# Performance work log

Hardware: AMD Instinct MI355X
Metric: run time of the kernel (lower is better)

The kernel has to match this reference:

```python
import jax, jax.numpy as jnp
import numpy as np

NUM_HEADS = 1
HIDDEN = 256
HEAD_DIM = HIDDEN // NUM_HEADS
SCALE = HEAD_DIM ** -0.5


def _rotate_pairwise(x):
    # (... , d) -> rotate adjacent pairs: (x0,x1,x2,x3,..) -> (-x1,x0,-x3,x2,..)
    shape = x.shape
    x = x.reshape(*shape[:-1], -1, 2)
    x = jnp.stack([-x[..., 1], x[..., 0]], axis=-1)
    return x.reshape(shape)


def setup_inputs() -> dict:
    key = jax.random.key(0)
    ks = jax.random.split(key, 12)
    B, PB, QS, KS = 1, 1, 4096, 16448
    KV_IN = 64
    d = {
        'query': jax.random.normal(ks[0], (B, PB, QS, HIDDEN), jnp.float32),
        'key': jax.random.normal(ks[1], (B, PB, KS, KV_IN), jnp.float32),
        'value': jax.random.normal(ks[2], (B, PB, KS, KV_IN), jnp.float32),
        'rope_cos': jax.random.normal(ks[3], (QS, HEAD_DIM), jnp.float32),
        'rope_sin': jax.random.normal(ks[4], (QS, HEAD_DIM), jnp.float32),
        'wq': jax.random.normal(ks[5], (HIDDEN, HIDDEN), jnp.float32) * (HIDDEN ** -0.5),
        'bq': jnp.zeros((HIDDEN,), jnp.float32),
        'wk': jax.random.normal(ks[6], (KV_IN, HIDDEN), jnp.float32) * (KV_IN ** -0.5),
        'bk': jnp.zeros((HIDDEN,), jnp.float32),
        'wv': jax.random.normal(ks[7], (KV_IN, HIDDEN), jnp.float32) * (KV_IN ** -0.5),
        'bv': jnp.zeros((HIDDEN,), jnp.float32),
        'wo': jax.random.normal(ks[8], (HIDDEN, HIDDEN), jnp.float32) * (HIDDEN ** -0.5),
        'bo': jnp.zeros((HIDDEN,), jnp.float32),
        'num_k_exclude_rope': 64,
    }
    return d


def reference(query, key, value, rope_cos, rope_sin, wq, bq, wk, bk, wv, bv, wo, bo, num_k_exclude_rope):
    batch, pb, qs, _ = query.shape
    ks = key.shape[2]
    B = batch * pb
    # projections -> [B, H, S, hd]
    q = (query @ wq + bq).reshape(B, qs, NUM_HEADS, HEAD_DIM).transpose(0, 2, 1, 3)
    k = (key @ wk + bk).reshape(B, ks, NUM_HEADS, HEAD_DIM).transpose(0, 2, 1, 3)
    v = (value @ wv + bv).reshape(B, ks, NUM_HEADS, HEAD_DIM).transpose(0, 2, 1, 3)
    cos = rope_cos[None, None]  # [1,1,QS,hd]
    sin = rope_sin[None, None]
    # split off non-RoPE keys (object pointer tokens)
    n_rot = ks - num_k_exclude_rope
    k_rot, k_pass = k[:, :, :n_rot, :], k[:, :, n_rot:, :]
    q = q * cos + _rotate_pairwise(q) * sin
    if n_rot != qs:  # rope_k_repeat branch (static shapes)
        rep = n_rot // qs
        cos_k = jnp.repeat(cos, rep, axis=2)
        sin_k = jnp.repeat(sin, rep, axis=2)
    else:
        cos_k, sin_k = cos, sin
    k_emb = k_rot * cos_k + _rotate_pairwise(k_rot) * sin_k
    k = jnp.concatenate([k_emb, k_pass], axis=-2)
    attn = jax.nn.softmax(jnp.einsum('bhqd,bhkd->bhqk', q * SCALE, k), axis=-1)
    x = jnp.einsum('bhqk,bhkd->bhqd', attn, v)
    x = x.transpose(0, 2, 1, 3).reshape(batch, pb, qs, HIDDEN)
    return x @ wo + bo
```

## Files before the change

### kernel.cpp

```cpp
#include <hip/hip_runtime.h>
#include <hip/hip_bf16.h>

typedef __attribute__((ext_vector_type(4))) float floatx4;
typedef __attribute__((ext_vector_type(8))) short shortx8;
typedef __attribute__((ext_vector_type(8))) _Float16 halfx8;
typedef _Float16 half_t;

#define MFMA_BF16(A,B,C) __builtin_amdgcn_mfma_f32_16x16x32_bf16((A),(B),(C),0,0,0)
#define GLOBAL_AS __attribute__((address_space(1)))
#define LDS_AS __attribute__((address_space(3)))

static __device__ __forceinline__ unsigned short f2b(float f) {
    union { float f; unsigned u; } v; v.f = f;
    unsigned r = v.u + 0x7FFFu + ((v.u >> 16) & 1u);
    return (unsigned short)(r >> 16);
}
static __device__ __forceinline__ unsigned pack_bf16(float lo, float hi) {
    return (unsigned)f2b(lo) | ((unsigned)f2b(hi) << 16);
}
static __device__ __forceinline__ unsigned pack_half(float lo, float hi) {
    union { half_t h[2]; unsigned u; } p;
    p.h[0] = (half_t)lo; p.h[1] = (half_t)hi;
    return p.u;
}
static __device__ __forceinline__ unsigned cvtpk_bf16(float lo, float hi) {
    unsigned r;
    asm("v_cvt_pk_bf16_f32 %0, %1, %2" : "=v"(r) : "v"(lo), "v"(hi));
    return r;
}
static __device__ __forceinline__ float EXP2F(float x) { return __builtin_amdgcn_exp2f(x); }

#define NSPLIT 8
#define NSPLIT_C 16
#define NTILES 257

__global__ __launch_bounds__(256) void wtrans_kernel(
    const float* __restrict__ wq, const float* __restrict__ wk,
    const float* __restrict__ wv, const float* __restrict__ wo,
    unsigned short* __restrict__ wqt, unsigned short* __restrict__ wkt,
    unsigned short* __restrict__ wvt, unsigned short* __restrict__ wot)
{
    __shared__ unsigned short tb[64 * 68];
    const int bid = blockIdx.x, tid = threadIdx.x;
    const float* src; unsigned short* dst; int K0, N0, Kfull;
    if (bid < 16)      { src = wq; dst = wqt; Kfull = 256; K0 = (bid >> 2) * 64; N0 = (bid & 3) * 64; }
    else if (bid < 20) { src = wk; dst = wkt; Kfull = 64;  K0 = 0; N0 = (bid - 16) * 64; }
    else if (bid < 24) { src = wv; dst = wvt; Kfull = 64;  K0 = 0; N0 = (bid - 20) * 64; }
    else { int t2 = bid - 24; src = wo; dst = wot; Kfull = 256; K0 = (t2 >> 2) * 64; N0 = (t2 & 3) * 64; }

    {
        const int r = tid >> 2, c0 = (tid & 3) * 16;
        const float* p = src + (K0 + r) * 256 + N0 + c0;
        #pragma unroll
        for (int j = 0; j < 16; j += 4) {
            floatx4 f = *(const floatx4*)(p + j);
            tb[r * 68 + c0 + j + 0] = f2b(f[0]);
            tb[r * 68 + c0 + j + 1] = f2b(f[1]);
            tb[r * 68 + c0 + j + 2] = f2b(f[2]);
            tb[r * 68 + c0 + j + 3] = f2b(f[3]);
        }
    }
    __syncthreads();
    {
        const int n = tid >> 2, k0 = (tid & 3) * 16;
        shortx8 v0, v1;
        #pragma unroll
        for (int j = 0; j < 8; j++) {
            v0[j] = tb[(k0 + j) * 68 + n];
            v1[j] = tb[(k0 + 8 + j) * 68 + n];
        }
        unsigned short* q = dst + (N0 + n) * Kfull + K0 + k0;
        *(shortx8*)q = v0;
        *(shortx8*)(q + 8) = v1;
    }
}

__global__ __launch_bounds__(256) void proj_kernel(
    const float* __restrict__ query, const float* __restrict__ key,
    const float* __restrict__ value,
    const unsigned short* __restrict__ wqt, const float* __restrict__ bq,
    const unsigned short* __restrict__ wkt, const float* __restrict__ bk,
    const unsigned short* __restrict__ wvt, const float* __restrict__ bv,
    const float* __restrict__ cosb, const float* __restrict__ sinb,
    const int* __restrict__ nkx,
    unsigned short* __restrict__ qr, unsigned short* __restrict__ krw,
    unsigned short* __restrict__ vtg)
{
    __shared__ unsigned short tbuf[256 * 72];
    const int tid = threadIdx.x;
    const int wave = tid >> 6, lane = tid & 63;
    const int c = lane & 15, quad = lane >> 4;
    const int bx = blockIdx.x;

    if (bx < 64) {
        const int m0 = bx * 64;
        shortx8 aA[8];
        {
            const int mrow = m0 + wave * 16 + c;
            #pragma unroll
            for (int ks = 0; ks < 8; ks++) {
                const float* p = query + mrow * 256 + ks * 32 + quad * 8;
                floatx4 f0 = *(const floatx4*)p;
                floatx4 f1 = *(const floatx4*)(p + 4);
                shortx8 a;
                #pragma unroll
                for (int j = 0; j < 4; j++) { a[j] = (short)f2b(f0[j]); a[j + 4] = (short)f2b(f1[j]); }
                aA[ks] = a;
            }
        }
        floatx4 acc[16];
        #pragma unroll
        for (int nt = 0; nt < 16; nt++) { acc[nt][0]=0.f; acc[nt][1]=0.f; acc[nt][2]=0.f; acc[nt][3]=0.f; }
        #pragma unroll
        for (int nt = 0; nt < 16; nt++) {
            #pragma unroll
            for (int ks = 0; ks < 8; ks++) {
                shortx8 b = *(const shortx8*)(wqt + (nt * 16 + c) * 256 + ks * 32 + quad * 8);
                acc[nt] = MFMA_BF16(aA[ks], b, acc[nt]);
            }
        }
        const float sc = 0.09016844005556021f;
        #pragma unroll
        for (int nt = 0; nt < 16; nt++) {
            const int col = nt * 16 + c;
            float vals[4];
            #pragma unroll
            for (int r = 0; r < 4; r++) {
                const int row = m0 + wave * 16 + quad * 4 + r;
                float v = acc[nt][r] + bq[col];
                float partner = __shfl_xor(v, 1);
                float cv = cosb[row * 256 + col];
                float sn = sinb[row * 256 + col];
                float rot = (col & 1) ? partner : -partner;
                vals[r] = (v * cv + rot * sn) * sc;
            }
            #pragma unroll
            for (int r2 = 0; r2 < 4; r2 += 2) {
                float a = vals[r2], b = vals[r2 + 1];
                float ax = __shfl_xor(a, 1), bx2 = __shfl_xor(b, 1);
                float lo = (c & 1) ? bx2 : a;
                float hi = (c & 1) ? b : ax;
                int row = m0 + wave * 16 + quad * 4 + r2 + (c & 1);
                *(unsigned*)(qr + row * 256 + nt * 16 + (c & ~1)) = pack_bf16(lo, hi);
            }
        }
        return;
    }

    const int isv = (bx >= 321);
    const int m0 = (isv ? (bx - 321) : (bx - 64)) * 64;
    const float* src = isv ? value : key;
    const unsigned short* wt = isv ? wvt : wkt;
    const float* bias = isv ? bv : bk;

    shortx8 aA[2];
    {
        const int mrow = m0 + wave * 16 + c;
        #pragma unroll
        for (int ks = 0; ks < 2; ks++) {
            const float* p = src + mrow * 64 + ks * 32 + quad * 8;
            floatx4 f0 = *(const floatx4*)p;
            floatx4 f1 = *(const floatx4*)(p + 4);
            shortx8 a;
            #pragma unroll
            for (int j = 0; j < 4; j++) { a[j] = (short)f2b(f0[j]); a[j + 4] = (short)f2b(f1[j]); }
            aA[ks] = a;
        }
    }
    floatx4 acc[16];
    #pragma unroll
    for (int nt = 0; nt < 16; nt++) { acc[nt][0]=0.f; acc[nt][1]=0.f; acc[nt][2]=0.f; acc[nt][3]=0.f; }
    #pragma unroll
    for (int nt = 0; nt < 16; nt++) {
        #pragma unroll
        for (int ks = 0; ks < 2; ks++) {
            shortx8 b = *(const shortx8*)(wt + (nt * 16 + c) * 64 + ks * 32 + quad * 8);
            acc[nt] = MFMA_BF16(aA[ks], b, acc[nt]);
        }
    }
    if (!isv) {
        const int n_rot = 16448 - nkx[0];
        int rep = n_rot / 4096; if (rep < 1) rep = 1;
        int rc4[4];
        #pragma unroll
        for (int r = 0; r < 4; r++) {
            int row = m0 + wave * 16 + quad * 4 + r;
            rc4[r] = row / rep;
        }
        #pragma unroll
        for (int nt = 0; nt < 16; nt++) {
            const int col = nt * 16 + c;
            float vals[4];
            #pragma unroll
            for (int r = 0; r < 4; r++) {
                const int row = m0 + wave * 16 + quad * 4 + r;
                float v = acc[nt][r] + bias[col];
                float partner = __shfl_xor(v, 1);
                float outv = v;
                if (row < n_rot) {
                    float cv = cosb[rc4[r] * 256 + col];
                    float sn = sinb[rc4[r] * 256 + col];
                    float rot = (col & 1) ? partner : -partner;
                    outv = v * cv + rot * sn;
                }
                vals[r] = outv;
            }
            #pragma unroll
            for (int r2 = 0; r2 < 4; r2 += 2) {
                float a = vals[r2], b = vals[r2 + 1];
                float ax = __shfl_xor(a, 1), bx2 = __shfl_xor(b, 1);
                float lo = (c & 1) ? bx2 : a;
                float hi = (c & 1) ? b : ax;
                int row = m0 + wave * 16 + quad * 4 + r2 + (c & 1);
                *(unsigned*)(krw + row * 256 + nt * 16 + (c & ~1)) = pack_bf16(lo, hi);
            }
        }
    } else {
        #pragma unroll
        for (int nt = 0; nt < 16; nt++) {
            const int col = nt * 16 + c;
            #pragma unroll
            for (int r = 0; r < 4; r++) {
                const int rl = wave * 16 + quad * 4 + r;
                tbuf[col * 72 + rl] = f2b(acc[nt][r] + bias[col]);
            }
        }
        __syncthreads();
        #pragma unroll
        for (int i = 0; i < 8; i++) {
            int G = i * 256 + tid;
            int n = G >> 3, g = G & 7;
            *(floatx4*)(vtg + n * 16448 + m0 + g * 8) = *(const floatx4*)(tbuf + n * 72 + g * 8);
        }
    }
}

__global__ __launch_bounds__(512, 2) void flash_kernel(
    const unsigned short* __restrict__ qr, const unsigned short* __restrict__ kr,
    const unsigned short* __restrict__ vt, half_t* __restrict__ Opart,
    float* __restrict__ Lpart)
{
    __shared__ unsigned short smem[65536];
    const int tid = threadIdx.x;
    const int wave = tid >> 6, lane = tid & 63;
    const int c = lane & 15, quad = lane >> 4;
    const int cx = c & 7;
    const int qg = wave & 3, kvh = wave >> 2;
    const int s = blockIdx.x & 7;
    const int xb = blockIdx.x >> 3;
    const int qrow0 = xb * 128 + qg * 32;
    const int t0 = (s * NTILES) / NSPLIT, t1 = ((s + 1) * NTILES) / NSPLIT;

    shortx8 aQ[2][8];
    #pragma unroll
    for (int u = 0; u < 2; u++)
        #pragma unroll
        for (int ks = 0; ks < 8; ks++)
            aQ[u][ks] = *(const shortx8*)(qr + (qrow0 + u * 16 + c) * 256 + ks * 32 + quad * 8);

    floatx4 o[2][16];
    #pragma unroll
    for (int u = 0; u < 2; u++)
        #pragma unroll
        for (int nt = 0; nt < 16; nt++) { o[u][nt][0]=0.f; o[u][nt][1]=0.f; o[u][nt][2]=0.f; o[u][nt][3]=0.f; }
    float l_i[2] = { 0.f, 0.f };

    auto stage = [&](int t, int buf) {
        const int kv0 = t * 64;
        unsigned short* kb = smem + buf * 16384;
        unsigned short* vb = smem + 32768 + buf * 16384;
        #pragma unroll
        for (int i = 0; i < 4; i++) {
            int L = i * 512 + tid;
            int kv = L >> 5, p = L & 31;
            int g = (p & 24) | ((p & 7) ^ ((kv >> 1) & 7));
            __builtin_amdgcn_global_load_lds(
                (const GLOBAL_AS void*)(const void*)(kr + (kv0 + kv) * 256 + g * 8),
                (LDS_AS void*)(void*)(kb + (i * 512 + wave * 64) * 8), 16, 0, 0);
        }
        #pragma unroll
        for (int i = 0; i < 4; i++) {
            int L = i * 512 + tid;
            int d = L >> 3, p = L & 7;
            int g = p ^ (d & 7);
            __builtin_amdgcn_global_load_lds(
                (const GLOBAL_AS void*)(const void*)(vt + d * 16448 + kv0 + g * 8),
                (LDS_AS void*)(void*)(vb + (i * 512 + wave * 64) * 8), 16, 0, 0);
        }
    };

    stage(t0, 0);
    int cur = 0;
    const int pv_p = (kvh * 4 + quad) ^ cx;
    for (int t = t0; t < t1; t++) {
        __syncthreads();
        if (t + 1 < t1) stage(t + 1, cur ^ 1);
        const unsigned short* kb = smem + cur * 16384;
        const unsigned short* vb = smem + 32768 + cur * 16384;

        floatx4 sv[2][2];
        #pragma unroll
        for (int u = 0; u < 2; u++)
            #pragma unroll
            for (int nt = 0; nt < 2; nt++) { sv[u][nt][0]=0.f; sv[u][nt][1]=0.f; sv[u][nt][2]=0.f; sv[u][nt][3]=0.f; }
        #pragma unroll
        for (int nt = 0; nt < 2; nt++) {
            const unsigned short* krow = kb + (kvh * 32 + 2 * c + nt) * 256;
            #pragma unroll
            for (int ks = 0; ks < 8; ks++) {
                int p = ((ks >> 1) * 8) | ((((ks & 1) << 2) + quad) ^ cx);
                shortx8 kfrag = *(const shortx8*)(krow + p * 8);
                sv[0][nt] = MFMA_BF16(kfrag, aQ[0][ks], sv[0][nt]);
                sv[1][nt] = MFMA_BF16(kfrag, aQ[1][ks], sv[1][nt]);
            }
        }
        #pragma unroll
        for (int u = 0; u < 2; u++) {
            float rs = 0.f;
            #pragma unroll
            for (int nt = 0; nt < 2; nt++)
                #pragma unroll
                for (int r = 0; r < 4; r++) {
                    float pv = EXP2F(sv[u][nt][r]);
                    sv[u][nt][r] = pv;
                    rs += pv;
                }
            l_i[u] += rs;
        }
        shortx8 aP[2];
        #pragma unroll
        for (int u = 0; u < 2; u++) {
            union { unsigned u4[4]; shortx8 v; } pk;
            #pragma unroll
            for (int m = 0; m < 4; m++)
                pk.u4[m] = cvtpk_bf16(sv[u][0][m], sv[u][1][m]);
            aP[u] = pk.v;
        }
        #pragma unroll
        for (int nt = 0; nt < 16; nt++) {
            const unsigned short* vrow = vb + (nt * 16 + c) * 64;
            shortx8 b0 = *(const shortx8*)(vrow + pv_p * 8);
            o[0][nt] = MFMA_BF16(aP[0], b0, o[0][nt]);
            o[1][nt] = MFMA_BF16(aP[1], b0, o[1][nt]);
        }
        cur ^= 1;
    }
    const int sEff = s * 2 + kvh;
    half_t* Ob = Opart + (size_t)sEff * (4096 * 256);
    #pragma unroll
    for (int u = 0; u < 2; u++) {
        l_i[u] += __shfl_xor(l_i[u], 16);
        l_i[u] += __shfl_xor(l_i[u], 32);
    }
    float inv[2] = { 1.0f / l_i[0], 1.0f / l_i[1] };
    #pragma unroll
    for (int u = 0; u < 2; u++) {
        float ar[4];
        #pragma unroll
        for (int r = 0; r < 4; r++) ar[r] = __shfl(inv[u], quad * 4 + r);
        #pragma unroll
        for (int nt = 0; nt < 16; nt++) {
            o[u][nt][0] *= ar[0]; o[u][nt][1] *= ar[1];
            o[u][nt][2] *= ar[2]; o[u][nt][3] *= ar[3];
        }
    }
    #pragma unroll
    for (int u = 0; u < 2; u++)
        #pragma unroll
        for (int nt = 0; nt < 16; nt++)
            #pragma unroll
            for (int r2 = 0; r2 < 4; r2 += 2) {
                float a = o[u][nt][r2], b = o[u][nt][r2 + 1];
                float ax = __shfl_xor(a, 1), bx2 = __shfl_xor(b, 1);
                float lo = (c & 1) ? bx2 : a;
                float hi = (c & 1) ? b : ax;
                int row = qrow0 + u * 16 + quad * 4 + r2 + (c & 1);
                *(unsigned*)(Ob + row * 256 + nt * 16 + (c & ~1)) = pack_half(lo, hi);
            }
    if (quad == 0) {
        #pragma unroll
        for (int u = 0; u < 2; u++)
            Lpart[sEff * 4096 + qrow0 + u * 16 + c] = l_i[u];
    }
}

__global__ __launch_bounds__(256) void combine_oproj_kernel(
    const half_t* __restrict__ Opart, const float* __restrict__ Lpart,
    const unsigned short* __restrict__ wot, const float* __restrict__ bo,
    float* __restrict__ outp)
{
    __shared__ unsigned short xt[16 * 264];
    const int tid = threadIdx.x;
    const int m0 = blockIdx.x * 16;

    {
        const int d0 = (tid & 31) * 8;
        #pragma unroll
        for (int pass = 0; pass < 2; pass++) {
            const int rl = pass * 8 + (tid >> 5);
            const int row = m0 + rl;
            float wn[NSPLIT_C], den = 0.f;
            #pragma unroll
            for (int sp = 0; sp < NSPLIT_C; sp++) { wn[sp] = Lpart[sp * 4096 + row]; den += wn[sp]; }
            float inv = 1.0f / den;
            float acc[8];
            #pragma unroll
            for (int j = 0; j < 8; j++) acc[j] = 0.f;
            #pragma unroll
            for (int sp = 0; sp < NSPLIT_C; sp++) {
                halfx8 hv = *(const halfx8*)(Opart + (size_t)sp * (4096 * 256) + row * 256 + d0);
                float w = wn[sp] * inv;
                #pragma unroll
                for (int j = 0; j < 8; j++) acc[j] += w * (float)hv[j];
            }
            shortx8 xv;
            #pragma unroll
            for (int j = 0; j < 8; j++) xv[j] = (short)f2b(acc[j]);
            *(shortx8*)(xt + rl * 264 + d0) = xv;
        }
    }
    __syncthreads();

    const int lane = tid & 63, wave = tid >> 6;
    const int c = lane & 15, quad = lane >> 4;
    shortx8 aX[8];
    #pragma unroll
    for (int ks = 0; ks < 8; ks++)
        aX[ks] = *(const shortx8*)(xt + c * 264 + ks * 32 + quad * 8);
    floatx4 acc[4];
    #pragma unroll
    for (int nt = 0; nt < 4; nt++) { acc[nt][0]=0.f; acc[nt][1]=0.f; acc[nt][2]=0.f; acc[nt][3]=0.f; }
    #pragma unroll
    for (int nt = 0; nt < 4; nt++) {
        const int n = (wave * 4 + nt) * 16;
        #pragma unroll
        for (int ks = 0; ks < 8; ks++) {
            shortx8 b = *(const shortx8*)(wot + (n + c) * 256 + ks * 32 + quad * 8);
            acc[nt] = MFMA_BF16(aX[ks], b, acc[nt]);
        }
    }
    #pragma unroll
    for (int nt = 0; nt < 4; nt++) {
        const int col = (wave * 4 + nt) * 16 + c;
        #pragma unroll
        for (int r = 0; r < 4; r++) {
            const int row = m0 + quad * 4 + r;
            outp[row * 256 + col] = acc[nt][r] + bo[col];
        }
    }
}

extern "C" void kernel_launch(void* const* d_in, const int* in_sizes, int n_in,
                              void* d_out, int out_size, void* d_ws, size_t ws_size,
                              hipStream_t stream) {
    const float* query = (const float*)d_in[0];
    const float* key   = (const float*)d_in[1];
    const float* value = (const float*)d_in[2];
    const float* cosb  = (const float*)d_in[3];
    const float* sinb  = (const float*)d_in[4];
    const float* wq    = (const float*)d_in[5];
    const float* bq    = (const float*)d_in[6];
    const float* wk    = (const float*)d_in[7];
    const float* bk    = (const float*)d_in[8];
    const float* wv    = (const float*)d_in[9];
    const float* bv    = (const float*)d_in[10];
    const float* wo    = (const float*)d_in[11];
    const float* bo    = (const float*)d_in[12];
    const int*   nk    = (const int*)d_in[13];

    char* ws = (char*)d_ws;
    unsigned short* wqt = (unsigned short*)(ws + 0);
    unsigned short* wkt = (unsigned short*)(ws + 131072);
    unsigned short* wvt = (unsigned short*)(ws + 163840);
    unsigned short* wot = (unsigned short*)(ws + 196608);
    unsigned short* qr  = (unsigned short*)(ws + 327680);
    unsigned short* krw = (unsigned short*)(ws + 2424832);
    unsigned short* vtg = (unsigned short*)(ws + 10846208);
    half_t* Opart = (half_t*)(ws + 19267584);
    float* Lpart = (float*)(ws + 52822016);
    float* outp  = (float*)d_out;

    wtrans_kernel<<<dim3(40), dim3(256), 0, stream>>>(wq, wk, wv, wo, wqt, wkt, wvt, wot);
    proj_kernel<<<dim3(578), dim3(256), 0, stream>>>(
        query, key, value, wqt, bq, wkt, bk, wvt, bv, cosb, sinb, nk, qr, krw, vtg);
    flash_kernel<<<dim3(256), dim3(512), 0, stream>>>(qr, krw, vtg, Opart, Lpart);
    combine_oproj_kernel<<<dim3(256), dim3(256), 0, stream>>>(Opart, Lpart, wot, bo, outp);
}
```

Before: 225.5 us.

## Merge the two KV-half partial outputs in LDS inside the flash kernel

Previously each of the two KV halves in a flash block wrote its own fp16 partial output and row sum to global memory, which gave 16 splits for the combine kernel to reduce. Now the kvh=1 warps stage their normalized partial O and l in shared memory, and the kvh=0 warps blend them in registers before writing a single partial per split. This halves the partial-output traffic written by the flash kernel and read by the combine kernel. The cost is two extra block barriers, an LDS round trip, and reuse of the K/V smem buffer, which must be large enough and no longer in use.

```diff
diff --git a/kernel.cpp b/kernel.cpp
--- a/kernel.cpp
+++ b/kernel.cpp
@@ -31,7 +31,7 @@
 static __device__ __forceinline__ float EXP2F(float x) { return __builtin_amdgcn_exp2f(x); }
 
 #define NSPLIT 8
-#define NSPLIT_C 16
+#define NSPLIT_C 8
 #define NTILES 257
 
 __global__ __launch_bounds__(256) void wtrans_kernel(
@@ -345,42 +345,70 @@
         }
         cur ^= 1;
     }
-    const int sEff = s * 2 + kvh;
-    half_t* Ob = Opart + (size_t)sEff * (4096 * 256);
+
     #pragma unroll
     for (int u = 0; u < 2; u++) {
         l_i[u] += __shfl_xor(l_i[u], 16);
         l_i[u] += __shfl_xor(l_i[u], 32);
     }
-    float inv[2] = { 1.0f / l_i[0], 1.0f / l_i[1] };
-    #pragma unroll
-    for (int u = 0; u < 2; u++) {
-        float ar[4];
-        #pragma unroll
-        for (int r = 0; r < 4; r++) ar[r] = __shfl(inv[u], quad * 4 + r);
-        #pragma unroll
-        for (int nt = 0; nt < 16; nt++) {
-            o[u][nt][0] *= ar[0]; o[u][nt][1] *= ar[1];
-            o[u][nt][2] *= ar[2]; o[u][nt][3] *= ar[3];
-        }
-    }
-    #pragma unroll
-    for (int u = 0; u < 2; u++)
-        #pragma unroll
-        for (int nt = 0; nt < 16; nt++)
-            #pragma unroll
-            for (int r2 = 0; r2 < 4; r2 += 2) {
-                float a = o[u][nt][r2], b = o[u][nt][r2 + 1];
-                float ax = __shfl_xor(a, 1), bx2 = __shfl_xor(b, 1);
-                float lo = (c & 1) ? bx2 : a;
-                float hi = (c & 1) ? b : ax;
-                int row = qrow0 + u * 16 + quad * 4 + r2 + (c & 1);
-                *(unsigned*)(Ob + row * 256 + nt * 16 + (c & ~1)) = pack_half(lo, hi);
-            }
-    if (quad == 0) {
-        #pragma unroll
-        for (int u = 0; u < 2; u++)
-            Lpart[sEff * 4096 + qrow0 + u * 16 + c] = l_i[u];
+    __syncthreads();
+    half_t* osh = (half_t*)smem;
+    float*  lsh = (float*)(smem + 32768);
+    if (kvh == 1) {
+        float inv1[2] = { 1.0f / l_i[0], 1.0f / l_i[1] };
+        #pragma unroll
+        for (int u = 0; u < 2; u++) {
+            float ar[4];
+            #pragma unroll
+            for (int r = 0; r < 4; r++) ar[r] = __shfl(inv1[u], quad * 4 + r);
+            #pragma unroll
+            for (int nt = 0; nt < 16; nt++) {
+                unsigned* dst = (unsigned*)(osh + (size_t)(((qg * 2 + u) * 16 + nt) * 64 + lane) * 4);
+                dst[0] = pack_half(o[u][nt][0] * ar[0], o[u][nt][1] * ar[1]);
+                dst[1] = pack_half(o[u][nt][2] * ar[2], o[u][nt][3] * ar[3]);
+            }
+            lsh[(qg * 2 + u) * 64 + lane] = l_i[u];
+        }
+    }
+    __syncthreads();
+    if (kvh == 0) {
+        half_t* Ob = Opart + (size_t)s * (4096 * 256);
+        float aI[2][4], aW[2][4];
+        #pragma unroll
+        for (int u = 0; u < 2; u++) {
+            float l1 = lsh[(qg * 2 + u) * 64 + lane];
+            float lt = l_i[u] + l1;
+            float inv = 1.0f / lt;
+            float w1 = l1 * inv;
+            if (quad == 0) Lpart[s * 4096 + qrow0 + u * 16 + c] = lt;
+            #pragma unroll
+            for (int r = 0; r < 4; r++) {
+                aI[u][r] = __shfl(inv, quad * 4 + r);
+                aW[u][r] = __shfl(w1, quad * 4 + r);
+            }
+        }
+        #pragma unroll
+        for (int u = 0; u < 2; u++) {
+            #pragma unroll
+            for (int nt = 0; nt < 16; nt++) {
+                const half_t* src = osh + (size_t)(((qg * 2 + u) * 16 + nt) * 64 + lane) * 4;
+                o[u][nt][0] = o[u][nt][0] * aI[u][0] + (float)src[0] * aW[u][0];
+                o[u][nt][1] = o[u][nt][1] * aI[u][1] + (float)src[1] * aW[u][1];
+                o[u][nt][2] = o[u][nt][2] * aI[u][2] + (float)src[2] * aW[u][2];
+                o[u][nt][3] = o[u][nt][3] * aI[u][3] + (float)src[3] * aW[u][3];
+            }
+            #pragma unroll
+            for (int nt = 0; nt < 16; nt++)
+                #pragma unroll
+                for (int r2 = 0; r2 < 4; r2 += 2) {
+                    float a = o[u][nt][r2], b = o[u][nt][r2 + 1];
+                    float ax = __shfl_xor(a, 1), bx2 = __shfl_xor(b, 1);
+                    float lo = (c & 1) ? bx2 : a;
+                    float hi = (c & 1) ? b : ax;
+                    int row = qrow0 + u * 16 + quad * 4 + r2 + (c & 1);
+                    *(unsigned*)(Ob + row * 256 + nt * 16 + (c & ~1)) = pack_half(lo, hi);
+                }
+        }
     }
 }
 
@@ -399,7 +427,8 @@
         for (int pass = 0; pass < 2; pass++) {
             const int rl = pass * 8 + (tid >> 5);
             const int row = m0 + rl;
-            float wn[NSPLIT_C], den = 0.f;
+            float den = 0.f;
+            float wn[NSPLIT_C];
             #pragma unroll
             for (int sp = 0; sp < NSPLIT_C; sp++) { wn[sp] = Lpart[sp * 4096 + row]; den += wn[sp]; }
             float inv = 1.0f / den;
@@ -477,7 +506,7 @@
     unsigned short* krw = (unsigned short*)(ws + 2424832);
     unsigned short* vtg = (unsigned short*)(ws + 10846208);
     half_t* Opart = (half_t*)(ws + 19267584);
-    float* Lpart = (float*)(ws + 52822016);
+    float* Lpart = (float*)(ws + 36044800);
     float* outp  = (float*)d_out;
 
     wtrans_kernel<<<dim3(40), dim3(256), 0, stream>>>(wq, wk, wv, wo, wqt, wkt, wvt, wot);
```

After: 222.6 us, median of 2. About the same (-1.3%).
